# Kernel tuning notes

Measured on AMD Instinct MI355X. Metric: run time of the kernel, lower is better.

The kernel has to match this reference:

```python
import jax, jax.numpy as jnp
import numpy as np

N = 50000      # nodes
E = 800000     # edges (avg degree 16)
HID = 64       # hidden / out_channels per head (concat=False)
EDIM = 3       # edge_dim
H = 4          # heads
C = 64         # per-head channels (== hidden since concat=False mean)
L = 2          # ode_layers
NEG_SLOPE = 0.2
LN_EPS = 1e-5


def setup_inputs() -> dict:
    key = jax.random.key(0)
    ks = jax.random.split(key, 12)
    h = jax.random.normal(ks[0], (N, HID), dtype=jnp.float32)
    edge_index = jax.random.randint(ks[1], (2, E), 0, N, dtype=jnp.int64)
    edge_attr = jax.random.normal(ks[2], (E, EDIM), dtype=jnp.float32)
    t = jnp.zeros((), dtype=jnp.float32)
    s = 1.0 / np.sqrt(HID)
    lin_W = jax.random.normal(ks[3], (L, H * C, HID), dtype=jnp.float32) * s
    lin_W = lin_W.at[L - 1].mul(0.1)  # mimics gats[-1].lin.weight.mul_(0.1)
    lin_edge_W = jax.random.normal(ks[4], (L, H * C, EDIM), dtype=jnp.float32) * (1.0 / np.sqrt(EDIM))
    att_src = jax.random.normal(ks[5], (L, H, C), dtype=jnp.float32) * s
    att_dst = jax.random.normal(ks[6], (L, H, C), dtype=jnp.float32) * s
    att_edge = jax.random.normal(ks[7], (L, H, C), dtype=jnp.float32) * s
    bias = jnp.zeros((L, C), dtype=jnp.float32)
    ln_gamma = jnp.ones((L, HID), dtype=jnp.float32)
    ln_beta = jnp.zeros((L, HID), dtype=jnp.float32)
    return {"t": t, "h": h, "edge_index": edge_index, "edge_attr": edge_attr,
            "lin_W": lin_W, "lin_edge_W": lin_edge_W, "att_src": att_src,
            "att_dst": att_dst, "att_edge": att_edge, "bias": bias,
            "ln_gamma": ln_gamma, "ln_beta": ln_beta}


def _gat_layer(z, src, dst, lin_W, lin_edge_W, att_src, att_dst, att_edge,
               bias, edge_attr):
    n = z.shape[0]
    x = (z @ lin_W.T).reshape(n, H, C)                      # [N,H,C]
    a_src = (x * att_src).sum(-1)                            # [N,H]
    a_dst = (x * att_dst).sum(-1)                            # [N,H]
    e = (edge_attr @ lin_edge_W.T).reshape(-1, H, C)         # [E,H,C]
    a_e = (e * att_edge).sum(-1)                             # [E,H]
    alpha = jax.nn.leaky_relu(a_src[src] + a_dst[dst] + a_e, NEG_SLOPE)
    # segment-softmax over incoming edges of each destination node
    amax = jax.ops.segment_max(alpha, dst, num_segments=n)
    amax = jnp.where(jnp.isfinite(amax), amax, 0.0)
    ex = jnp.exp(alpha - amax[dst])                          # [E,H]
    denom = jax.ops.segment_sum(ex, dst, num_segments=n)
    w = ex / (denom[dst] + 1e-16)
    msg = jax.ops.segment_sum(w[:, :, None] * x[src], dst, num_segments=n)
    return msg.mean(axis=1) + bias                           # [N,C] (concat=False)


def reference(t, h, edge_index, edge_attr, lin_W, lin_edge_W, att_src,
              att_dst, att_edge, bias, ln_gamma, ln_beta):
    src, dst = edge_index[0], edge_index[1]
    z = h
    for i in range(L):
        out = _gat_layer(z, src, dst, lin_W[i], lin_edge_W[i], att_src[i],
                         att_dst[i], att_edge[i], bias[i], edge_attr)
        mu = out.mean(-1, keepdims=True)
        var = ((out - mu) ** 2).mean(-1, keepdims=True)
        ln = (out - mu) / jnp.sqrt(var + LN_EPS) * ln_gamma[i] + ln_beta[i]
        z = jax.nn.silu(ln)
    return z
```

## Files before the change

kernel.cpp:

```cpp
#include <hip/hip_runtime.h>
#include <math.h>

#define NN 50000
#define NE 800000
#define NEG_SLOPE 0.2f
#define LN_EPS 1e-5f
#define SROW 264

typedef unsigned short ushort_t;
typedef unsigned int uint_t;
typedef __attribute__((ext_vector_type(8))) short bf16x8;
typedef __attribute__((ext_vector_type(4))) float f32x4;

__device__ __forceinline__ float bf2f(ushort_t u) {
    return __uint_as_float(((uint_t)u) << 16);
}
__device__ __forceinline__ ushort_t f2bf(float f) {
    uint_t b = __float_as_uint(f);
    uint_t r = (b + 0x7fffu + ((b >> 16) & 1u)) >> 16;
    return (ushort_t)r;
}
__device__ __forceinline__ float ldx(const void* p, size_t i, int isbf) {
    return isbf ? bf2f(((const ushort_t*)p)[i]) : ((const float*)p)[i];
}
__device__ __forceinline__ int clampN(int v) {
    return v < 0 ? 0 : (v >= NN ? NN - 1 : v);
}
__device__ __forceinline__ int sniff_f64(const int* ei) {
    return (ei[1] == 0 && ei[3] == 0 && ei[5] == 0 && ei[7] == 0) ? 1 : 0;
}

__global__ __launch_bounds__(256) void setup(
    const void* __restrict__ lin_W, const void* __restrict__ lin_edge_W,
    const void* __restrict__ att_src, const void* __restrict__ att_dst,
    const void* __restrict__ att_edge, const void* __restrict__ h_in,
    const int* __restrict__ ei, float* __restrict__ Mbuf,
    ushort_t* __restrict__ wext, int* __restrict__ esrc, int* __restrict__ edst,
    int* __restrict__ deg, int* __restrict__ flags) {
    int tid = threadIdx.x, lane = tid & 63;
    int nthreads = gridDim.x * 256;
    int gtid = blockIdx.x * 256 + tid;
    __shared__ int s_bf;
    if (tid == 0) s_bf = 1;
    __syncthreads();
    {
        uint_t ex = (((const ushort_t*)h_in)[2 * tid] >> 7) & 0xFFu;
        if (ex > 0x8Cu) s_bf = 0;
    }
    __syncthreads();
    int isbf = s_bf;
    int f64 = sniff_f64(ei);
    if (gtid == 0) {
        flags[0] = f64;
        flags[1] = isbf;
    }
    for (int i = gtid; i < NN; i += nthreads) deg[i] = 0;
    if (f64) {
        const int4* s4 = (const int4*)ei;
        const int4* d4 = (const int4*)(ei + 2 * NE);
        for (int p = gtid; p < NE / 2; p += nthreads) {
            int4 sv = s4[p], dv = d4[p];
            esrc[2 * p]     = clampN(sv.x);
            esrc[2 * p + 1] = clampN(sv.z);
            edst[2 * p]     = clampN(dv.x);
            edst[2 * p + 1] = clampN(dv.z);
        }
    } else {
        const int2* s2 = (const int2*)ei;
        const int2* d2 = (const int2*)(ei + NE);
        for (int p = gtid; p < NE / 2; p += nthreads) {
            int2 sv = s2[p], dv = d2[p];
            esrc[2 * p]     = clampN(sv.x);
            esrc[2 * p + 1] = clampN(sv.y);
            edst[2 * p]     = clampN(dv.x);
            edst[2 * p + 1] = clampN(dv.y);
        }
    }
    if (blockIdx.x == 0) {
        for (int rep = 0; rep < 2; ++rep) {
            int idx = rep * 256 + tid;
            int l = idx >> 8, hc = idx & 255;
            float ae = ldx(att_edge, l * 256 + hc, isbf);
            size_t b3 = ((size_t)l * 256 + hc) * 3;
            float q0 = ae * ldx(lin_edge_W, b3 + 0, isbf);
            float q1 = ae * ldx(lin_edge_W, b3 + 1, isbf);
            float q2 = ae * ldx(lin_edge_W, b3 + 2, isbf);
            for (int off = 32; off > 0; off >>= 1) {
                q0 += __shfl_down(q0, off);
                q1 += __shfl_down(q1, off);
                q2 += __shfl_down(q2, off);
            }
            if (lane == 0) {
                int h = (idx >> 6) & 3;
                Mbuf[(l * 4 + h) * 3 + 0] = q0;
                Mbuf[(l * 4 + h) * 3 + 1] = q1;
                Mbuf[(l * 4 + h) * 3 + 2] = q2;
            }
        }
    }
    for (int idx = gtid; idx < 2 * 272 * 64; idx += nthreads) {
        int d = idx & 63;
        int row = (idx >> 6) % 272;
        int l = idx / (272 * 64);
        float v = 0.f;
        if (row < 256) {
            v = ldx(lin_W, ((size_t)l * 256 + row) * 64 + d, isbf);
        } else if (row < 264) {
            int h = (row - 256) & 3;
            const void* att = (row < 260) ? att_src : att_dst;
            for (int c = 0; c < 64; ++c) {
                v += ldx(lin_W, ((size_t)l * 256 + h * 64 + c) * 64 + d, isbf) *
                     ldx(att, l * 256 + h * 64 + c, isbf);
            }
        }
        wext[((size_t)l * 272 + row) * 64 + d] = f2bf(v);
    }
}


__global__ void csr_hist_pos(const int* __restrict__ edst, int* __restrict__ deg,
                             int* __restrict__ pos) {
    int e = blockIdx.x * 256 + threadIdx.x;
    if (e >= NE) return;
    pos[e] = atomicAdd(&deg[edst[e]], 1);
}

__global__ __launch_bounds__(1024) void csr_scan1(const int* __restrict__ deg,
                                                  int* __restrict__ rowptr,
                                                  int* __restrict__ bsum) {
    __shared__ int sh[1024];
    int i = blockIdx.x * 1024 + threadIdx.x;
    int v = (i < NN) ? deg[i] : 0;
    sh[threadIdx.x] = v;
    __syncthreads();
    for (int off = 1; off < 1024; off <<= 1) {
        int t = (threadIdx.x >= off) ? sh[threadIdx.x - off] : 0;
        __syncthreads();
        sh[threadIdx.x] += t;
        __syncthreads();
    }
    if (i < NN) rowptr[i] = sh[threadIdx.x] - v;
    if (threadIdx.x == 1023) bsum[blockIdx.x] = sh[1023];
}

__global__ __launch_bounds__(1024) void csr_scan23(int* __restrict__ rowptr,
                                                   const int* __restrict__ bsum,
                                                   int nb) {
    __shared__ int off_sh;
    int tid = threadIdx.x;
    if (tid < 64) {
        int v = (tid < blockIdx.x && tid < nb) ? bsum[tid] : 0;
        for (int off = 32; off > 0; off >>= 1) v += __shfl_down(v, off);
        if (tid == 0) off_sh = v;
    }
    __syncthreads();
    int i = blockIdx.x * 1024 + tid;
    if (i < NN) rowptr[i] += off_sh;
    if (i == 0) rowptr[NN] = NE;
}

__global__ void csr_fill(const int* __restrict__ esrc, const int* __restrict__ edst,
                         const void* __restrict__ edge_attr,
                         const int* __restrict__ rowptr, const int* __restrict__ pos,
                         float4* __restrict__ edata, const int* __restrict__ flags) {
    int e = blockIdx.x * 256 + threadIdx.x;
    if (e >= NE) return;
    int isbf = flags[1];
    int s = esrc[e], d = edst[e];
    float4 ed;
    ed.x = ldx(edge_attr, (size_t)e * 3 + 0, isbf);
    ed.y = ldx(edge_attr, (size_t)e * 3 + 1, isbf);
    ed.z = ldx(edge_attr, (size_t)e * 3 + 2, isbf);
    ed.w = __int_as_float(s);
    edata[rowptr[d] + pos[e]] = ed;
}


__global__ __launch_bounds__(256) void node_linear(
    const void* __restrict__ h_in, const ushort_t* __restrict__ zbuf,
    const ushort_t* __restrict__ wext,
    ushort_t* __restrict__ xb, float* __restrict__ a_src, float* __restrict__ a_dst,
    const int* __restrict__ flags, int layer) {
    __shared__ __align__(16) ushort_t st_all[4 * 16 * SROW];
    int isbf = flags[1];
    int tid = threadIdx.x, wv = tid >> 6, lane = tid & 63;
    int q = lane >> 4, mi = lane & 15;
    int f32path = (layer == 0) && !isbf;
    const ushort_t* zsrc = (layer == 0) ? (const ushort_t*)h_in : zbuf;
    const ushort_t* wl = wext + (size_t)layer * 272 * 64;
    bf16x8 wf[34];
#pragma unroll
    for (int t = 0; t < 17; ++t) {
        const ushort_t* wrow = wl + (size_t)(t * 16 + mi) * 64;
        wf[2 * t]     = *(const bf16x8*)(wrow + q * 8);
        wf[2 * t + 1] = *(const bf16x8*)(wrow + 32 + q * 8);
    }
    ushort_t* st = st_all + wv * 16 * SROW;
    int gwave = blockIdx.x * 4 + wv, nwaves = gridDim.x * 4;
    for (int tile = gwave; tile < NN / 16; tile += nwaves) {
        int mbase = tile * 16, mynode = mbase + mi;
        bf16x8 b0, b1;
        if (f32path) {
            const float* zf = (const float*)h_in + (size_t)mynode * 64;
            float4 fa = *(const float4*)(zf + q * 8);
            float4 fb = *(const float4*)(zf + q * 8 + 4);
            float4 fc = *(const float4*)(zf + 32 + q * 8);
            float4 fd = *(const float4*)(zf + 32 + q * 8 + 4);
            b0[0] = (short)f2bf(fa.x); b0[1] = (short)f2bf(fa.y);
            b0[2] = (short)f2bf(fa.z); b0[3] = (short)f2bf(fa.w);
            b0[4] = (short)f2bf(fb.x); b0[5] = (short)f2bf(fb.y);
            b0[6] = (short)f2bf(fb.z); b0[7] = (short)f2bf(fb.w);
            b1[0] = (short)f2bf(fc.x); b1[1] = (short)f2bf(fc.y);
            b1[2] = (short)f2bf(fc.z); b1[3] = (short)f2bf(fc.w);
            b1[4] = (short)f2bf(fd.x); b1[5] = (short)f2bf(fd.y);
            b1[6] = (short)f2bf(fd.z); b1[7] = (short)f2bf(fd.w);
        } else {
            const ushort_t* zrow = zsrc + (size_t)mynode * 64;
            b0 = *(const bf16x8*)(zrow + q * 8);
            b1 = *(const bf16x8*)(zrow + 32 + q * 8);
        }
#pragma unroll
        for (int t = 0; t < 17; ++t) {
            f32x4 acc = {0.f, 0.f, 0.f, 0.f};
            acc = __builtin_amdgcn_mfma_f32_16x16x32_bf16(wf[2 * t], b0, acc, 0, 0, 0);
            acc = __builtin_amdgcn_mfma_f32_16x16x32_bf16(wf[2 * t + 1], b1, acc, 0, 0, 0);
            if (t < 16) {
                ushort4 pk;
                pk.x = f2bf(acc[0]);
                pk.y = f2bf(acc[1]);
                pk.z = f2bf(acc[2]);
                pk.w = f2bf(acc[3]);
                *(ushort4*)(st + mi * SROW + t * 16 + q * 4) = pk;
            } else {
                float4 av;
                av.x = acc[0]; av.y = acc[1]; av.z = acc[2]; av.w = acc[3];
                if (q == 0) *(float4*)(a_src + (size_t)mynode * 4) = av;
                else if (q == 1) *(float4*)(a_dst + (size_t)mynode * 4) = av;
            }
        }
        for (int nn = 0; nn < 16; ++nn) {
            int node = mbase + nn;
            ushort4 pk;
            pk.x = st[nn * SROW + lane];
            pk.y = st[nn * SROW + 64 + lane];
            pk.z = st[nn * SROW + 128 + lane];
            pk.w = st[nn * SROW + 192 + lane];
            *(ushort4*)(xb + (size_t)node * 256 + lane * 4) = pk;
        }
    }
}

__global__ __launch_bounds__(256) void node_aggregate(
    const int* __restrict__ rowptr, const float4* __restrict__ edata,
    const float* __restrict__ a_src, const float* __restrict__ a_dst,
    const ushort_t* __restrict__ xb, const float* __restrict__ Mbuf,
    const void* __restrict__ bias, const void* __restrict__ gamma,
    const void* __restrict__ beta, ushort_t* __restrict__ zout,
    void* __restrict__ outp, const int* __restrict__ flags, int layer, int last) {
    __shared__ float4 wsh[4][64];
    __shared__ int ssh[4][64];
    int isbf = flags[1];
    int wv = threadIdx.x >> 6;
    int lane = threadIdx.x & 63;
    int n = blockIdx.x * 4 + wv;
    float M[12];
#pragma unroll
    for (int i = 0; i < 12; ++i) M[i] = Mbuf[layer * 12 + i];
    float4 ad = *(const float4*)(a_dst + (size_t)n * 4);
    int start = rowptr[n], end = rowptr[n + 1];
    float acc0 = 0.f, acc1 = 0.f, acc2 = 0.f, acc3 = 0.f;
    float den0 = 0.f, den1 = 0.f, den2 = 0.f, den3 = 0.f;
    for (int cb = start; cb < end; cb += 64) {
        int m = end - cb;
        if (m > 64) m = 64;
        if (lane < m) {
            float4 ed = edata[cb + lane];
            int s = __float_as_int(ed.w);
            float4 as4 = *(const float4*)(a_src + (size_t)s * 4);
            float t0 = as4.x + ad.x + ed.x * M[0] + ed.y * M[1] + ed.z * M[2];
            float t1 = as4.y + ad.y + ed.x * M[3] + ed.y * M[4] + ed.z * M[5];
            float t2 = as4.z + ad.z + ed.x * M[6] + ed.y * M[7] + ed.z * M[8];
            float t3 = as4.w + ad.w + ed.x * M[9] + ed.y * M[10] + ed.z * M[11];
            t0 = t0 > 0.f ? t0 : NEG_SLOPE * t0;
            t1 = t1 > 0.f ? t1 : NEG_SLOPE * t1;
            t2 = t2 > 0.f ? t2 : NEG_SLOPE * t2;
            t3 = t3 > 0.f ? t3 : NEG_SLOPE * t3;
            float4 ex;
            ex.x = __expf(fminf(t0, 80.f));
            ex.y = __expf(fminf(t1, 80.f));
            ex.z = __expf(fminf(t2, 80.f));
            ex.w = __expf(fminf(t3, 80.f));
            wsh[wv][lane] = ex;
            ssh[wv][lane] = s;
        }
        for (int j = 0; j < m; j += 4) {
            int j1 = j + 1 < m ? j + 1 : m - 1;
            int j2 = j + 2 < m ? j + 2 : m - 1;
            int j3 = j + 3 < m ? j + 3 : m - 1;
            int s0 = ssh[wv][j],  s1 = ssh[wv][j1];
            int s2 = ssh[wv][j2], s3 = ssh[wv][j3];
            float4 w0 = wsh[wv][j];
            float4 w1 = wsh[wv][j1];
            float4 w2 = wsh[wv][j2];
            float4 w3 = wsh[wv][j3];
            if (j + 1 >= m) w1 = make_float4(0.f, 0.f, 0.f, 0.f);
            if (j + 2 >= m) w2 = make_float4(0.f, 0.f, 0.f, 0.f);
            if (j + 3 >= m) w3 = make_float4(0.f, 0.f, 0.f, 0.f);
            ushort4 x0 = *(const ushort4*)(xb + (size_t)s0 * 256 + lane * 4);
            ushort4 x1 = *(const ushort4*)(xb + (size_t)s1 * 256 + lane * 4);
            ushort4 x2 = *(const ushort4*)(xb + (size_t)s2 * 256 + lane * 4);
            ushort4 x3 = *(const ushort4*)(xb + (size_t)s3 * 256 + lane * 4);
            acc0 += w0.x * bf2f(x0.x) + w1.x * bf2f(x1.x) +
                    w2.x * bf2f(x2.x) + w3.x * bf2f(x3.x);
            acc1 += w0.y * bf2f(x0.y) + w1.y * bf2f(x1.y) +
                    w2.y * bf2f(x2.y) + w3.y * bf2f(x3.y);
            acc2 += w0.z * bf2f(x0.z) + w1.z * bf2f(x1.z) +
                    w2.z * bf2f(x2.z) + w3.z * bf2f(x3.z);
            acc3 += w0.w * bf2f(x0.w) + w1.w * bf2f(x1.w) +
                    w2.w * bf2f(x2.w) + w3.w * bf2f(x3.w);
            den0 += w0.x + w1.x + w2.x + w3.x;
            den1 += w0.y + w1.y + w2.y + w3.y;
            den2 += w0.z + w1.z + w2.z + w3.z;
            den3 += w0.w + w1.w + w2.w + w3.w;
        }
    }
    float v = ldx(bias, layer * 64 + lane, isbf) +
              0.25f * (acc0 / (den0 + 1e-16f) + acc1 / (den1 + 1e-16f) +
                       acc2 / (den2 + 1e-16f) + acc3 / (den3 + 1e-16f));
    float sum = v;
    for (int off = 1; off < 64; off <<= 1) sum += __shfl_xor(sum, off);
    float mu = sum * (1.f / 64.f);
    float d = v - mu;
    float vv = d * d;
    for (int off = 1; off < 64; off <<= 1) vv += __shfl_xor(vv, off);
    float var = vv * (1.f / 64.f);
    float ln = d * rsqrtf(var + LN_EPS) * ldx(gamma, layer * 64 + lane, isbf) +
               ldx(beta, layer * 64 + lane, isbf);
    float sl = ln / (1.f + __expf(-ln));
    size_t idx = (size_t)n * 64 + lane;
    if (last) {
        if (isbf) ((ushort_t*)outp)[idx] = f2bf(sl);
        else      ((float*)outp)[idx] = sl;
    } else {
        zout[idx] = f2bf(sl);
    }
}

extern "C" void kernel_launch(void* const* d_in, const int* in_sizes, int n_in,
                              void* d_out, int out_size, void* d_ws, size_t ws_size,
                              hipStream_t stream) {
    int off = (in_sizes[0] == 1) ? 1 : 0;
    const void* h_in  = d_in[off + 0];
    const int*  ei    = (const int*)d_in[off + 1];
    const void* eattr = d_in[off + 2];
    const void* linW  = d_in[off + 3];
    const void* linEW = d_in[off + 4];
    const void* attS  = d_in[off + 5];
    const void* attD  = d_in[off + 6];
    const void* attE  = d_in[off + 7];
    const void* bias  = d_in[off + 8];
    const void* gamma = d_in[off + 9];
    const void* beta  = d_in[off + 10];

    char* w = (char*)d_ws;
    size_t o = 0;
    auto alloc = [&](size_t bytes) {
        void* q = w + o;
        o += (bytes + 255) & ~(size_t)255;
        return q;
    };
    int*    flags  = (int*)alloc(8);
    float*  Mbuf   = (float*)alloc(24 * 4);
    ushort_t* wext = (ushort_t*)alloc((size_t)2 * 272 * 64 * 2);
    float*  a_src  = (float*)alloc((size_t)NN * 4 * 4);
    float*  a_dst  = (float*)alloc((size_t)NN * 4 * 4);
    int*    rowptr = (int*)alloc((size_t)(NN + 1) * 4);
    int*    deg    = (int*)alloc((size_t)NN * 4);
    int*    pos    = (int*)alloc((size_t)NE * 4);
    int*    bsum   = (int*)alloc(256 * 4);
    ushort_t* zbuf = (ushort_t*)alloc((size_t)NN * 64 * 2);
    int*    esrc   = (int*)alloc((size_t)NE * 4);
    int*    edst   = (int*)alloc((size_t)NE * 4);
    ushort_t* xb   = (ushort_t*)alloc((size_t)NN * 256 * 2);
    float4* edata  = (float4*)alloc((size_t)NE * 16);

    int nb = (NN + 1023) / 1024;
    setup<<<256, 256, 0, stream>>>(linW, linEW, attS, attD, attE, h_in, ei,
                                   Mbuf, wext, esrc, edst, deg, flags);
    csr_hist_pos<<<(NE + 255) / 256, 256, 0, stream>>>(edst, deg, pos);
    csr_scan1<<<nb, 1024, 0, stream>>>(deg, rowptr, bsum);
    csr_scan23<<<nb, 1024, 0, stream>>>(rowptr, bsum, nb);
    csr_fill<<<(NE + 255) / 256, 256, 0, stream>>>(esrc, edst, eattr, rowptr,
                                                   pos, edata, flags);

    for (int l = 0; l < 2; ++l) {
        node_linear<<<512, 256, 0, stream>>>(h_in, zbuf, wext, xb,
                                             a_src, a_dst, flags, l);
        node_aggregate<<<NN / 4, 256, 0, stream>>>(rowptr, edata, a_src, a_dst,
                                                   xb, Mbuf, bias, gamma, beta,
                                                   zbuf, d_out, flags, l, l == 1);
    }
}
```

Before: 313.8 us.

## Fuse CSR histogram into setup and scan into layer-0 linear kernel

Moves the degree histogram and per-edge position atomics into the setup kernel and zeroes the degree array with a memset. The two-kernel scan becomes a single-block serial-chunk scan that runs as block 0 of the layer-0 linear kernel, while the other blocks do the projection concurrently. csr_fill is vectorised to handle four edges per thread, and the att-folded weight loop uses four partial accumulators. The goal is fewer kernel launches and less serialisation, at the cost of a slow single-block scan whose latency may now sit on the critical path.

New measurement: 323.4 us. +3.0%, slower.

```diff
diff --git a/kernel.cpp b/kernel.cpp
--- a/kernel.cpp
+++ b/kernel.cpp
@@ -36,7 +36,7 @@
     const void* __restrict__ att_edge, const void* __restrict__ h_in,
     const int* __restrict__ ei, float* __restrict__ Mbuf,
     ushort_t* __restrict__ wext, int* __restrict__ esrc, int* __restrict__ edst,
-    int* __restrict__ deg, int* __restrict__ flags) {
+    int* __restrict__ deg, int* __restrict__ pos, int* __restrict__ flags) {
     int tid = threadIdx.x, lane = tid & 63;
     int nthreads = gridDim.x * 256;
     int gtid = blockIdx.x * 256 + tid;
@@ -54,26 +54,31 @@
         flags[0] = f64;
         flags[1] = isbf;
     }
-    for (int i = gtid; i < NN; i += nthreads) deg[i] = 0;
     if (f64) {
         const int4* s4 = (const int4*)ei;
         const int4* d4 = (const int4*)(ei + 2 * NE);
         for (int p = gtid; p < NE / 2; p += nthreads) {
             int4 sv = s4[p], dv = d4[p];
+            int d0 = clampN(dv.x), d1 = clampN(dv.z);
             esrc[2 * p]     = clampN(sv.x);
             esrc[2 * p + 1] = clampN(sv.z);
-            edst[2 * p]     = clampN(dv.x);
-            edst[2 * p + 1] = clampN(dv.z);
+            edst[2 * p]     = d0;
+            edst[2 * p + 1] = d1;
+            pos[2 * p]      = atomicAdd(&deg[d0], 1);
+            pos[2 * p + 1]  = atomicAdd(&deg[d1], 1);
         }
     } else {
         const int2* s2 = (const int2*)ei;
         const int2* d2 = (const int2*)(ei + NE);
         for (int p = gtid; p < NE / 2; p += nthreads) {
             int2 sv = s2[p], dv = d2[p];
+            int d0 = clampN(dv.x), d1 = clampN(dv.y);
             esrc[2 * p]     = clampN(sv.x);
             esrc[2 * p + 1] = clampN(sv.y);
-            edst[2 * p]     = clampN(dv.x);
-            edst[2 * p + 1] = clampN(dv.y);
+            edst[2 * p]     = d0;
+            edst[2 * p + 1] = d1;
+            pos[2 * p]      = atomicAdd(&deg[d0], 1);
+            pos[2 * p + 1]  = atomicAdd(&deg[d1], 1);
         }
     }
     if (blockIdx.x == 0) {
@@ -108,86 +113,34 @@
         } else if (row < 264) {
             int h = (row - 256) & 3;
             const void* att = (row < 260) ? att_src : att_dst;
-            for (int c = 0; c < 64; ++c) {
-                v += ldx(lin_W, ((size_t)l * 256 + h * 64 + c) * 64 + d, isbf) *
-                     ldx(att, l * 256 + h * 64 + c, isbf);
+            float v0 = 0.f, v1 = 0.f, v2 = 0.f, v3 = 0.f;
+            for (int c = 0; c < 64; c += 4) {
+                size_t wb = ((size_t)l * 256 + h * 64 + c) * 64 + d;
+                size_t ab = (size_t)l * 256 + h * 64 + c;
+                v0 += ldx(lin_W, wb,       isbf) * ldx(att, ab,     isbf);
+                v1 += ldx(lin_W, wb + 64,  isbf) * ldx(att, ab + 1, isbf);
+                v2 += ldx(lin_W, wb + 128, isbf) * ldx(att, ab + 2, isbf);
+                v3 += ldx(lin_W, wb + 192, isbf) * ldx(att, ab + 3, isbf);
             }
+            v = (v0 + v1) + (v2 + v3);
         }
         wext[((size_t)l * 272 + row) * 64 + d] = f2bf(v);
     }
 }
 
 
-__global__ void csr_hist_pos(const int* __restrict__ edst, int* __restrict__ deg,
-                             int* __restrict__ pos) {
-    int e = blockIdx.x * 256 + threadIdx.x;
-    if (e >= NE) return;
-    pos[e] = atomicAdd(&deg[edst[e]], 1);
-}
-
-__global__ __launch_bounds__(1024) void csr_scan1(const int* __restrict__ deg,
-                                                  int* __restrict__ rowptr,
-                                                  int* __restrict__ bsum) {
-    __shared__ int sh[1024];
-    int i = blockIdx.x * 1024 + threadIdx.x;
-    int v = (i < NN) ? deg[i] : 0;
-    sh[threadIdx.x] = v;
-    __syncthreads();
-    for (int off = 1; off < 1024; off <<= 1) {
-        int t = (threadIdx.x >= off) ? sh[threadIdx.x - off] : 0;
-        __syncthreads();
-        sh[threadIdx.x] += t;
-        __syncthreads();
-    }
-    if (i < NN) rowptr[i] = sh[threadIdx.x] - v;
-    if (threadIdx.x == 1023) bsum[blockIdx.x] = sh[1023];
-}
-
-__global__ __launch_bounds__(1024) void csr_scan23(int* __restrict__ rowptr,
-                                                   const int* __restrict__ bsum,
-                                                   int nb) {
-    __shared__ int off_sh;
-    int tid = threadIdx.x;
-    if (tid < 64) {
-        int v = (tid < blockIdx.x && tid < nb) ? bsum[tid] : 0;
-        for (int off = 32; off > 0; off >>= 1) v += __shfl_down(v, off);
-        if (tid == 0) off_sh = v;
-    }
-    __syncthreads();
-    int i = blockIdx.x * 1024 + tid;
-    if (i < NN) rowptr[i] += off_sh;
-    if (i == 0) rowptr[NN] = NE;
-}
-
-__global__ void csr_fill(const int* __restrict__ esrc, const int* __restrict__ edst,
-                         const void* __restrict__ edge_attr,
-                         const int* __restrict__ rowptr, const int* __restrict__ pos,
-                         float4* __restrict__ edata, const int* __restrict__ flags) {
-    int e = blockIdx.x * 256 + threadIdx.x;
-    if (e >= NE) return;
-    int isbf = flags[1];
-    int s = esrc[e], d = edst[e];
-    float4 ed;
-    ed.x = ldx(edge_attr, (size_t)e * 3 + 0, isbf);
-    ed.y = ldx(edge_attr, (size_t)e * 3 + 1, isbf);
-    ed.z = ldx(edge_attr, (size_t)e * 3 + 2, isbf);
-    ed.w = __int_as_float(s);
-    edata[rowptr[d] + pos[e]] = ed;
-}
-
-
-__global__ __launch_bounds__(256) void node_linear(
-    const void* __restrict__ h_in, const ushort_t* __restrict__ zbuf,
-    const ushort_t* __restrict__ wext,
-    ushort_t* __restrict__ xb, float* __restrict__ a_src, float* __restrict__ a_dst,
-    const int* __restrict__ flags, int layer) {
+template <int LAYER>
+__device__ __forceinline__ void linear_body(
+    int bid, int nblk, const void* __restrict__ h_in,
+    const ushort_t* __restrict__ zbuf, const ushort_t* __restrict__ wext,
+    ushort_t* __restrict__ xb, float* __restrict__ a_src,
+    float* __restrict__ a_dst, int isbf) {
     __shared__ __align__(16) ushort_t st_all[4 * 16 * SROW];
-    int isbf = flags[1];
     int tid = threadIdx.x, wv = tid >> 6, lane = tid & 63;
     int q = lane >> 4, mi = lane & 15;
-    int f32path = (layer == 0) && !isbf;
-    const ushort_t* zsrc = (layer == 0) ? (const ushort_t*)h_in : zbuf;
-    const ushort_t* wl = wext + (size_t)layer * 272 * 64;
+    int f32path = (LAYER == 0) && !isbf;
+    const ushort_t* zsrc = (LAYER == 0) ? (const ushort_t*)h_in : zbuf;
+    const ushort_t* wl = wext + (size_t)LAYER * 272 * 64;
     bf16x8 wf[34];
 #pragma unroll
     for (int t = 0; t < 17; ++t) {
@@ -196,7 +149,7 @@
         wf[2 * t + 1] = *(const bf16x8*)(wrow + 32 + q * 8);
     }
     ushort_t* st = st_all + wv * 16 * SROW;
-    int gwave = blockIdx.x * 4 + wv, nwaves = gridDim.x * 4;
+    int gwave = bid * 4 + wv, nwaves = nblk * 4;
     for (int tile = gwave; tile < NN / 16; tile += nwaves) {
         int mbase = tile * 16, mynode = mbase + mi;
         bf16x8 b0, b1;
@@ -248,6 +201,86 @@
             *(ushort4*)(xb + (size_t)node * 256 + lane * 4) = pk;
         }
     }
+}
+
+__global__ __launch_bounds__(256) void scan_linear0(
+    const int* __restrict__ deg, int* __restrict__ rowptr,
+    const void* __restrict__ h_in, const ushort_t* __restrict__ wext,
+    ushort_t* __restrict__ xb, float* __restrict__ a_src,
+    float* __restrict__ a_dst, const int* __restrict__ flags) {
+    if (blockIdx.x == 0) {
+        __shared__ int sh[256];
+        int tid = threadIdx.x;
+        const int PER = 200;
+        int base = tid * PER;
+        int s = 0;
+        if (tid < 250) {
+            for (int i = 0; i < PER; ++i) s += deg[base + i];
+        }
+        sh[tid] = s;
+        __syncthreads();
+        for (int off = 1; off < 256; off <<= 1) {
+            int t = (tid >= off) ? sh[tid - off] : 0;
+            __syncthreads();
+            sh[tid] += t;
+            __syncthreads();
+        }
+        int excl = sh[tid] - s;
+        if (tid < 250) {
+            int run = excl;
+            for (int i = 0; i < PER; ++i) {
+                rowptr[base + i] = run;
+                run += deg[base + i];
+            }
+        }
+        if (tid == 255) rowptr[NN] = NE;
+    } else {
+        linear_body<0>(blockIdx.x - 1, gridDim.x - 1, h_in, (const ushort_t*)0,
+                       wext, xb, a_src, a_dst, flags[1]);
+    }
+}
+
+__global__ __launch_bounds__(256) void node_linear1(
+    const ushort_t* __restrict__ zbuf, const ushort_t* __restrict__ wext,
+    ushort_t* __restrict__ xb, float* __restrict__ a_src,
+    float* __restrict__ a_dst, const int* __restrict__ flags) {
+    linear_body<1>(blockIdx.x, gridDim.x, (const void*)0, zbuf, wext, xb,
+                   a_src, a_dst, flags[1]);
+}
+
+__global__ void csr_fill(const int* __restrict__ esrc, const int* __restrict__ edst,
+                         const void* __restrict__ edge_attr,
+                         const int* __restrict__ rowptr, const int* __restrict__ pos,
+                         float4* __restrict__ edata, const int* __restrict__ flags) {
+    int e4 = blockIdx.x * 256 + threadIdx.x;
+    if (e4 >= NE / 4) return;
+    int isbf = flags[1];
+    int e = e4 * 4;
+    int4 sv = *(const int4*)(esrc + e);
+    int4 dv = *(const int4*)(edst + e);
+    int4 pv = *(const int4*)(pos + e);
+    float a[12];
+    if (!isbf) {
+        const float4* ea = (const float4*)((const float*)edge_attr + (size_t)e * 3);
+        float4 f0 = ea[0], f1 = ea[1], f2 = ea[2];
+        a[0] = f0.x; a[1] = f0.y; a[2]  = f0.z;
+        a[3] = f0.w; a[4] = f1.x; a[5]  = f1.y;
+        a[6] = f1.z; a[7] = f1.w; a[8]  = f2.x;
+        a[9] = f2.y; a[10] = f2.z; a[11] = f2.w;
+    } else {
+#pragma unroll
+        for (int i = 0; i < 12; ++i)
+            a[i] = bf2f(((const ushort_t*)edge_attr)[(size_t)e * 3 + i]);
+    }
+    float4 ed0, ed1, ed2, ed3;
+    ed0.x = a[0]; ed0.y = a[1];  ed0.z = a[2];  ed0.w = __int_as_float(sv.x);
+    ed1.x = a[3]; ed1.y = a[4];  ed1.z = a[5];  ed1.w = __int_as_float(sv.y);
+    ed2.x = a[6]; ed2.y = a[7];  ed2.z = a[8];  ed2.w = __int_as_float(sv.z);
+    ed3.x = a[9]; ed3.y = a[10]; ed3.z = a[11]; ed3.w = __int_as_float(sv.w);
+    edata[rowptr[dv.x] + pv.x] = ed0;
+    edata[rowptr[dv.y] + pv.y] = ed1;
+    edata[rowptr[dv.z] + pv.z] = ed2;
+    edata[rowptr[dv.w] + pv.w] = ed3;
 }
 
 __global__ __launch_bounds__(256) void node_aggregate(
@@ -377,27 +410,24 @@
     int*    rowptr = (int*)alloc((size_t)(NN + 1) * 4);
     int*    deg    = (int*)alloc((size_t)NN * 4);
     int*    pos    = (int*)alloc((size_t)NE * 4);
-    int*    bsum   = (int*)alloc(256 * 4);
     ushort_t* zbuf = (ushort_t*)alloc((size_t)NN * 64 * 2);
     int*    esrc   = (int*)alloc((size_t)NE * 4);
     int*    edst   = (int*)alloc((size_t)NE * 4);
     ushort_t* xb   = (ushort_t*)alloc((size_t)NN * 256 * 2);
     float4* edata  = (float4*)alloc((size_t)NE * 16);
 
-    int nb = (NN + 1023) / 1024;
+    hipMemsetAsync(deg, 0, (size_t)NN * 4, stream);
     setup<<<256, 256, 0, stream>>>(linW, linEW, attS, attD, attE, h_in, ei,
-                                   Mbuf, wext, esrc, edst, deg, flags);
-    csr_hist_pos<<<(NE + 255) / 256, 256, 0, stream>>>(edst, deg, pos);
-    csr_scan1<<<nb, 1024, 0, stream>>>(deg, rowptr, bsum);
-    csr_scan23<<<nb, 1024, 0, stream>>>(rowptr, bsum, nb);
-    csr_fill<<<(NE + 255) / 256, 256, 0, stream>>>(esrc, edst, eattr, rowptr,
-                                                   pos, edata, flags);
-
-    for (int l = 0; l < 2; ++l) {
-        node_linear<<<512, 256, 0, stream>>>(h_in, zbuf, wext, xb,
-                                             a_src, a_dst, flags, l);
-        node_aggregate<<<NN / 4, 256, 0, stream>>>(rowptr, edata, a_src, a_dst,
-                                                   xb, Mbuf, bias, gamma, beta,
-                                                   zbuf, d_out, flags, l, l == 1);
-    }
-}
+                                   Mbuf, wext, esrc, edst, deg, pos, flags);
+    scan_linear0<<<513, 256, 0, stream>>>(deg, rowptr, h_in, wext, xb,
+                                          a_src, a_dst, flags);
+    csr_fill<<<(NE / 4 + 255) / 256, 256, 0, stream>>>(esrc, edst, eattr,
+                                                       rowptr, pos, edata, flags);
+    node_aggregate<<<NN / 4, 256, 0, stream>>>(rowptr, edata, a_src, a_dst,
+                                               xb, Mbuf, bias, gamma, beta,
+                                               zbuf, d_out, flags, 0, 0);
+    node_linear1<<<512, 256, 0, stream>>>(zbuf, wext, xb, a_src, a_dst, flags);
+    node_aggregate<<<NN / 4, 256, 0, stream>>>(rowptr, edata, a_src, a_dst,
+                                               xb, Mbuf, bias, gamma, beta,
+                                               zbuf, d_out, flags, 1, 1);
+}
```

## Fuse degree histogram into setup and collapse CSR scan into one kernel

Applied to the files above, without the earlier changes.

Computes per-edge slot positions with atomics on the destination degree inside the setup kernel, which removes the separate histogram kernel. The degree array is now zeroed with a memset so no in-kernel ordering hazard arises. The two-pass scan becomes a single kernel in which each block recomputes its prefix by summing all preceding degrees, trading redundant reads for fewer launches. Setup's grid is enlarged, and the attention-weight fold loop is unrolled into four independent accumulators.

Measured after the change: 318.4 us. Within noise of the previous version (+1.4%).

```diff
diff --git a/kernel.cpp b/kernel.cpp
--- a/kernel.cpp
+++ b/kernel.cpp
@@ -36,7 +36,7 @@
     const void* __restrict__ att_edge, const void* __restrict__ h_in,
     const int* __restrict__ ei, float* __restrict__ Mbuf,
     ushort_t* __restrict__ wext, int* __restrict__ esrc, int* __restrict__ edst,
-    int* __restrict__ deg, int* __restrict__ flags) {
+    int* __restrict__ deg, int* __restrict__ pos, int* __restrict__ flags) {
     int tid = threadIdx.x, lane = tid & 63;
     int nthreads = gridDim.x * 256;
     int gtid = blockIdx.x * 256 + tid;
@@ -54,26 +54,31 @@
         flags[0] = f64;
         flags[1] = isbf;
     }
-    for (int i = gtid; i < NN; i += nthreads) deg[i] = 0;
     if (f64) {
         const int4* s4 = (const int4*)ei;
         const int4* d4 = (const int4*)(ei + 2 * NE);
         for (int p = gtid; p < NE / 2; p += nthreads) {
             int4 sv = s4[p], dv = d4[p];
+            int d0 = clampN(dv.x), d1 = clampN(dv.z);
             esrc[2 * p]     = clampN(sv.x);
             esrc[2 * p + 1] = clampN(sv.z);
-            edst[2 * p]     = clampN(dv.x);
-            edst[2 * p + 1] = clampN(dv.z);
+            edst[2 * p]     = d0;
+            edst[2 * p + 1] = d1;
+            pos[2 * p]      = atomicAdd(&deg[d0], 1);
+            pos[2 * p + 1]  = atomicAdd(&deg[d1], 1);
         }
     } else {
         const int2* s2 = (const int2*)ei;
         const int2* d2 = (const int2*)(ei + NE);
         for (int p = gtid; p < NE / 2; p += nthreads) {
             int2 sv = s2[p], dv = d2[p];
+            int d0 = clampN(dv.x), d1 = clampN(dv.y);
             esrc[2 * p]     = clampN(sv.x);
             esrc[2 * p + 1] = clampN(sv.y);
-            edst[2 * p]     = clampN(dv.x);
-            edst[2 * p + 1] = clampN(dv.y);
+            edst[2 * p]     = d0;
+            edst[2 * p + 1] = d1;
+            pos[2 * p]      = atomicAdd(&deg[d0], 1);
+            pos[2 * p + 1]  = atomicAdd(&deg[d1], 1);
         }
     }
     if (blockIdx.x == 0) {
@@ -108,55 +113,49 @@
         } else if (row < 264) {
             int h = (row - 256) & 3;
             const void* att = (row < 260) ? att_src : att_dst;
-            for (int c = 0; c < 64; ++c) {
-                v += ldx(lin_W, ((size_t)l * 256 + h * 64 + c) * 64 + d, isbf) *
-                     ldx(att, l * 256 + h * 64 + c, isbf);
+            float v0 = 0.f, v1 = 0.f, v2 = 0.f, v3 = 0.f;
+            for (int c = 0; c < 64; c += 4) {
+                size_t wb = ((size_t)l * 256 + h * 64 + c) * 64 + d;
+                size_t ab = (size_t)l * 256 + h * 64 + c;
+                v0 += ldx(lin_W, wb,       isbf) * ldx(att, ab,     isbf);
+                v1 += ldx(lin_W, wb + 64,  isbf) * ldx(att, ab + 1, isbf);
+                v2 += ldx(lin_W, wb + 128, isbf) * ldx(att, ab + 2, isbf);
+                v3 += ldx(lin_W, wb + 192, isbf) * ldx(att, ab + 3, isbf);
             }
+            v = (v0 + v1) + (v2 + v3);
         }
         wext[((size_t)l * 272 + row) * 64 + d] = f2bf(v);
     }
 }
 
 
-__global__ void csr_hist_pos(const int* __restrict__ edst, int* __restrict__ deg,
-                             int* __restrict__ pos) {
-    int e = blockIdx.x * 256 + threadIdx.x;
-    if (e >= NE) return;
-    pos[e] = atomicAdd(&deg[edst[e]], 1);
-}
-
-__global__ __launch_bounds__(1024) void csr_scan1(const int* __restrict__ deg,
-                                                  int* __restrict__ rowptr,
-                                                  int* __restrict__ bsum) {
+__global__ __launch_bounds__(1024) void rowscan(const int* __restrict__ deg,
+                                                int* __restrict__ rowptr) {
     __shared__ int sh[1024];
-    int i = blockIdx.x * 1024 + threadIdx.x;
+    int tid = threadIdx.x;
+    int base = blockIdx.x * 1024;
+    int pre = 0;
+    for (int i = tid; i < base; i += 1024) pre += deg[i];
+    sh[tid] = pre;
+    __syncthreads();
+    for (int off = 512; off > 0; off >>= 1) {
+        if (tid < off) sh[tid] += sh[tid + off];
+        __syncthreads();
+    }
+    int blockoff = sh[0];
+    __syncthreads();
+    int i = base + tid;
     int v = (i < NN) ? deg[i] : 0;
-    sh[threadIdx.x] = v;
+    sh[tid] = v;
     __syncthreads();
     for (int off = 1; off < 1024; off <<= 1) {
-        int t = (threadIdx.x >= off) ? sh[threadIdx.x - off] : 0;
+        int t = (tid >= off) ? sh[tid - off] : 0;
         __syncthreads();
-        sh[threadIdx.x] += t;
+        sh[tid] += t;
         __syncthreads();
     }
-    if (i < NN) rowptr[i] = sh[threadIdx.x] - v;
-    if (threadIdx.x == 1023) bsum[blockIdx.x] = sh[1023];
-}
-
-__global__ __launch_bounds__(1024) void csr_scan23(int* __restrict__ rowptr,
-                                                   const int* __restrict__ bsum,
-                                                   int nb) {
-    __shared__ int off_sh;
-    int tid = threadIdx.x;
-    if (tid < 64) {
-        int v = (tid < blockIdx.x && tid < nb) ? bsum[tid] : 0;
-        for (int off = 32; off > 0; off >>= 1) v += __shfl_down(v, off);
-        if (tid == 0) off_sh = v;
-    }
-    __syncthreads();
-    int i = blockIdx.x * 1024 + tid;
-    if (i < NN) rowptr[i] += off_sh;
-    if (i == 0) rowptr[NN] = NE;
+    if (i < NN) rowptr[i] = blockoff + sh[tid] - v;
+    if (blockIdx.x == 0 && tid == 0) rowptr[NN] = NE;
 }
 
 __global__ void csr_fill(const int* __restrict__ esrc, const int* __restrict__ edst,
@@ -377,19 +376,16 @@
     int*    rowptr = (int*)alloc((size_t)(NN + 1) * 4);
     int*    deg    = (int*)alloc((size_t)NN * 4);
     int*    pos    = (int*)alloc((size_t)NE * 4);
-    int*    bsum   = (int*)alloc(256 * 4);
     ushort_t* zbuf = (ushort_t*)alloc((size_t)NN * 64 * 2);
     int*    esrc   = (int*)alloc((size_t)NE * 4);
     int*    edst   = (int*)alloc((size_t)NE * 4);
     ushort_t* xb   = (ushort_t*)alloc((size_t)NN * 256 * 2);
     float4* edata  = (float4*)alloc((size_t)NE * 16);
 
-    int nb = (NN + 1023) / 1024;
-    setup<<<256, 256, 0, stream>>>(linW, linEW, attS, attD, attE, h_in, ei,
-                                   Mbuf, wext, esrc, edst, deg, flags);
-    csr_hist_pos<<<(NE + 255) / 256, 256, 0, stream>>>(edst, deg, pos);
-    csr_scan1<<<nb, 1024, 0, stream>>>(deg, rowptr, bsum);
-    csr_scan23<<<nb, 1024, 0, stream>>>(rowptr, bsum, nb);
+    hipMemsetAsync(deg, 0, (size_t)NN * 4, stream);
+    setup<<<1024, 256, 0, stream>>>(linW, linEW, attS, attD, attE, h_in, ei,
+                                    Mbuf, wext, esrc, edst, deg, pos, flags);
+    rowscan<<<(NN + 1023) / 1024, 1024, 0, stream>>>(deg, rowptr);
     csr_fill<<<(NE + 255) / 256, 256, 0, stream>>>(esrc, edst, eattr, rowptr,
                                                    pos, edata, flags);
 
```
